# Kernel optimization log

Measured on AMD Instinct MI355X. Metric: run time of the kernel, lower is better.

The kernel has to match this reference:

```python
import jax, jax.numpy as jnp
import numpy as np

B, L, D, N_HEADS = 4, 8192, 1024, 16
HD = D // N_HEADS
MASK_NEG = -1e10


def setup_inputs() -> dict:
    key = jax.random.key(0)
    ks = jax.random.split(key, 5)
    # xavier_normal std for square Dense: sqrt(2/(fan_in+fan_out))
    std = (2.0 / (D + D)) ** 0.5
    return {
        "query": jax.random.normal(ks[0], (B, L, D), dtype=jnp.float32),
        "mask": jax.random.bernoulli(ks[1], 0.1, (B, L)),  # True = masked out
        "Wq": std * jax.random.normal(ks[2], (D, D), dtype=jnp.float32),
        "bq": jnp.zeros((D,), dtype=jnp.float32),
        "Wk": std * jax.random.normal(ks[3], (D, D), dtype=jnp.float32),
        "bk": jnp.zeros((D,), dtype=jnp.float32),
        "Wv": std * jax.random.normal(ks[4], (D, D), dtype=jnp.float32),
        "bv": jnp.zeros((D,), dtype=jnp.float32),
    }


def reference(query, mask, Wq, bq, Wk, bk, Wv, bv):
    # Self-attention: key = value = query (original falls back when key/value are None)
    q = query @ Wq + bq  # [B, L, D]
    k = query @ Wk + bk
    v = query @ Wv + bv
    # split heads: b l (n h) -> b l n h
    qs = q.reshape(B, L, N_HEADS, HD)
    ks_ = k.reshape(B, L, N_HEADS, HD)
    vs = v.reshape(B, L, N_HEADS, HD)
    m = mask[:, :, None, None]  # [B, L, 1, 1], broadcast over heads & dims
    K = jnp.where(m, MASK_NEG, ks_)
    V = jnp.where(m, 0.0, vs)
    # elu kernel feature map: phi(x) = elu(x) + 1 (elu(-1e10)+1 -> 0 for masked keys)
    phiK = jax.nn.elu(K) + 1.0
    phiQ = jax.nn.elu(qs) + 1.0
    # per-head kv summary: [B, N, HD_k, HD_v]
    kv = jnp.einsum('blnk,blnv->bnkv', phiK, V)
    # FAITHFUL to original einsum 'blk,bkv->blk': sums kv over v, elementwise with phiQ
    kv_sum = kv.sum(-1)  # [B, N, HD]
    out = phiQ * kv_sum[:, None, :, :]  # [B, L, N, HD]
    # combine heads: b l n h -> b l (n h)
    return out.reshape(B, L, D)
```

## Files before the change

### kernel.cpp

```cpp
#include <hip/hip_runtime.h>

typedef unsigned short u16;
typedef unsigned int u32;
typedef __attribute__((ext_vector_type(8))) short s16x8;
typedef __attribute__((ext_vector_type(4))) float f32x4;

#define GAS __attribute__((address_space(1)))
#define LAS __attribute__((address_space(3)))

#define BB 4
#define LL 8192
#define DD 1024
#define NH 16
#define HD 64
#define MROWS (BB * LL)
#define NWBT 2064

__device__ __forceinline__ u16 f2bf(float f) {
  u32 u = __builtin_bit_cast(u32, f);
  u32 r = (u + 0x7FFFu + ((u >> 16) & 1u)) >> 16;
  return (u16)r;
}
__device__ __forceinline__ float bf2f(u32 lo) {
  return __builtin_bit_cast(float, lo << 16);
}

__device__ __forceinline__ void async16(const void* g, void* l) {
  __builtin_amdgcn_global_load_lds((const GAS u32*)g, (LAS u32*)l, 16, 0, 0);
}

__device__ __forceinline__ bool get_mask(const void* mp, int row, int mode) {
  if (mode == 2) return ((const unsigned char*)mp)[row] != 0;
  if (mode == 1) return ((const float*)mp)[row] != 0.f;
  return ((const int*)mp)[row] != 0;
}

__global__ void detect_mask(const u32* __restrict__ m, int* __restrict__ flag) {
  int i = blockIdx.x * 256 + threadIdx.x;
  u32 v = m[i];
  int f = 0;
  if (v == 0x3F800000u) f = 1;
  else if (v > 1u) f = 2;
  if (f) atomicMax(flag, f);
}

__global__ void build_wbt(const float* __restrict__ Wq, const float* __restrict__ Wk,
                          u16* __restrict__ WbT) {
  __shared__ float t[32][33];
  const int n0 = blockIdx.x * 32;
  const int k0 = blockIdx.y * 32;
  const float* W = (n0 >> 10) == 0 ? Wq : Wk;
  const int nloc = n0 & 1023;
  const int tx = threadIdx.x, ty = threadIdx.y;
#pragma unroll
  for (int j = 0; j < 32; j += 8)
    t[ty + j][tx] = W[(size_t)(k0 + ty + j) * DD + nloc + tx];
  __syncthreads();
#pragma unroll
  for (int j = 0; j < 32; j += 8)
    WbT[(size_t)(n0 + ty + j) * DD + k0 + tx] = f2bf(t[tx][ty + j]);
}

__global__ void build_wvs(const float* __restrict__ Wv, u16* __restrict__ WbT) {
  int i = blockIdx.x * 256 + threadIdx.x;
  int k = i >> 4, h = i & 15;
  float s = 0.f;
  const float* p = Wv + (size_t)k * DD + h * HD;
#pragma unroll 8
  for (int j = 0; j < 64; ++j) s += p[j];
  WbT[(size_t)(2048 + h) * DD + k] = f2bf(s);
}

__global__ void build_bcat(const float* __restrict__ bq, const float* __restrict__ bk,
                           const float* __restrict__ bv, float* __restrict__ bcat) {
  int i = blockIdx.x * 256 + threadIdx.x;
  if (i < 1024) bcat[i] = bq[i];
  else if (i < 2048) bcat[i] = bk[i - 1024];
  else if (i < 2064) {
    float s = 0.f;
    const float* p = bv + (i - 2048) * HD;
#pragma unroll 8
    for (int j = 0; j < 64; ++j) s += p[j];
    bcat[i] = s;
  }
}

__global__ __launch_bounds__(256) void prep_q(
    const float* __restrict__ query, const u16* __restrict__ WbT,
    const float* __restrict__ bcat, const void* __restrict__ maskp,
    const int* __restrict__ mmode,
    u16* __restrict__ qb, float* __restrict__ sV) {
  __shared__ u16 ldsW[16 * 1024];
  __shared__ u16 ldsA[128 * 64];
  const int tid = threadIdx.x;
  const int lane = tid & 63;
  const int w = tid >> 6;
  const int row0 = blockIdx.x * 128;

  {
    const int h = tid & 15;
    const int cb = tid >> 4;
#pragma unroll
    for (int j = 0; j < 8; ++j) {
      const int c = cb * 8 + j;
      s16x8 v = *(const s16x8*)(WbT + (size_t)(2048 + h) * DD + c * 8);
      *(s16x8*)(ldsW + h * 1024 + (c ^ (h & 7)) * 8) = v;
    }
  }

  const int r_l = tid >> 3;
  const int slot = tid & 7;
  f32x4 acc[2] = {};

  for (int k0 = 0; k0 < DD; k0 += 64) {
    __syncthreads();
#pragma unroll
    for (int i = 0; i < 4; ++i) {
      const int rl = i * 32 + r_l;
      const int seg = slot ^ (rl & 7);
      const float* gp = query + (size_t)(row0 + rl) * DD + k0 + seg * 8;
      float4 v0 = *(const float4*)gp;
      float4 v1 = *(const float4*)(gp + 4);
      s16x8 o;
      o[0] = (short)f2bf(v0.x); o[1] = (short)f2bf(v0.y);
      o[2] = (short)f2bf(v0.z); o[3] = (short)f2bf(v0.w);
      o[4] = (short)f2bf(v1.x); o[5] = (short)f2bf(v1.y);
      o[6] = (short)f2bf(v1.z); o[7] = (short)f2bf(v1.w);
      *(s16x8*)(qb + (size_t)(row0 + rl) * DD + k0 + seg * 8) = o;
      *(s16x8*)(ldsA + rl * 64 + slot * 8) = o;
    }
    __syncthreads();
#pragma unroll
    for (int kk = 0; kk < 2; ++kk) {
      const int segk = kk * 4 + (lane >> 4);
      const int hh = lane & 15;
      const int cc = (k0 >> 3) + segk;
      s16x8 bfr = *(const s16x8*)(ldsW + hh * 1024 + (cc ^ (hh & 7)) * 8);
#pragma unroll
      for (int mi = 0; mi < 2; ++mi) {
        const int r = w * 32 + mi * 16 + hh;
        s16x8 af = *(const s16x8*)(ldsA + r * 64 + ((segk ^ (r & 7))) * 8);
        acc[mi] = __builtin_amdgcn_mfma_f32_16x16x32_bf16(af, bfr, acc[mi], 0, 0, 0);
      }
    }
  }

  const int mode = *mmode;
  const int lanec = lane & 15, laneq = lane >> 4;
#pragma unroll
  for (int mi = 0; mi < 2; ++mi)
#pragma unroll
    for (int r = 0; r < 4; ++r) {
      const int row = row0 + w * 32 + mi * 16 + laneq * 4 + r;
      const bool msk = get_mask(maskp, row, mode);
      float v = acc[mi][r] + bcat[2048 + lanec];
      sV[(size_t)row * NH + lanec] = msk ? 0.f : v;
    }
}

#define BUFSZ 8192
#define UOFF(buf, mat, ks) (((((buf)*2 + (mat))*2 + (ks))) * BUFSZ)

__global__ __launch_bounds__(512, 2) void gemm_qkv(
    const u16* __restrict__ qb, const u16* __restrict__ WbT,
    const float* __restrict__ bcat, const void* __restrict__ maskp,
    const int* __restrict__ mmode,
    const float* __restrict__ sV, float* __restrict__ kv,
    float* __restrict__ out, int phase) {
  __shared__ __align__(16) u16 lds[65536];
  const int tid = threadIdx.x;
  const int lane = tid & 63;
  const int w = tid >> 6;
  const int wm = w & 1, wn = w >> 1;
  const int l15 = lane & 15, l16 = lane >> 4;

  const int bid = blockIdx.x;
  const int swz = (bid & 7) * 64 + (bid >> 3);
  const int mt = swz >> 2;
  const int nt = swz & 3;
  const int row0 = mt * 256;
  const int col0 = (phase ? 1024 : 0) + nt * 256;

  f32x4 acc[8][4] = {};

#define STAGE(buf, mat, ks, kt) do {                                        \
    const u16* gb_ = (mat) ? (WbT + (size_t)col0 * DD)                      \
                           : (qb + (size_t)row0 * DD);                      \
    const int kt_ = (kt) & 15;                                              \
    _Pragma("unroll")                                                       \
    for (int j_ = 0; j_ < 2; ++j_) {                                        \
      int li_ = tid + j_ * 512;                                             \
      int row_ = li_ >> 2, slot_ = li_ & 3;                                 \
      int c_ = slot_ ^ ((row_ >> 1) & 3);                                   \
      async16(gb_ + (size_t)row_ * DD + kt_ * 64 + (ks) * 32 + c_ * 8,      \
              lds + UOFF(buf, mat, ks) + li_ * 8);                          \
    }                                                                       \
  } while (0)

#define LDA(buf, ks, a) do {                                                \
    _Pragma("unroll")                                                       \
    for (int mi_ = 0; mi_ < 8; ++mi_) {                                     \
      int r_ = wm * 128 + mi_ * 16 + l15;                                   \
      a[mi_] = *(const s16x8*)(lds + UOFF(buf, 0, ks) + r_ * 32 +           \
                               ((l16 ^ ((r_ >> 1) & 3)) * 8));              \
    }                                                                       \
  } while (0)

#define LDB2(buf, ks, nb, b) do {                                           \
    _Pragma("unroll")                                                       \
    for (int q_ = 0; q_ < 2; ++q_) {                                        \
      int r_ = wn * 64 + ((nb)*2 + q_) * 16 + l15;                          \
      b[q_] = *(const s16x8*)(lds + UOFF(buf, 1, ks) + r_ * 32 +            \
                              ((l16 ^ ((r_ >> 1) & 3)) * 8));               \
    }                                                                       \
  } while (0)

#define MM(a, b, nb) do {                                                   \
    __builtin_amdgcn_s_setprio(1);                                          \
    _Pragma("unroll")                                                       \
    for (int mi_ = 0; mi_ < 8; ++mi_) {                                     \
      acc[mi_][(nb)*2] = __builtin_amdgcn_mfma_f32_16x16x32_bf16(           \
          a[mi_], b[0], acc[mi_][(nb)*2], 0, 0, 0);                         \
      acc[mi_][(nb)*2 + 1] = __builtin_amdgcn_mfma_f32_16x16x32_bf16(       \
          a[mi_], b[1], acc[mi_][(nb)*2 + 1], 0, 0, 0);                     \
    }                                                                       \
    __builtin_amdgcn_s_setprio(0);                                          \
  } while (0)

#define BAR() __builtin_amdgcn_s_barrier()
#define VMW6() asm volatile("s_waitcnt vmcnt(6)" ::: "memory")

  STAGE(0, 0, 0, 0); STAGE(0, 1, 0, 0); STAGE(0, 0, 1, 0); STAGE(0, 1, 1, 0);
  STAGE(1, 0, 0, 1); STAGE(1, 1, 0, 1); STAGE(1, 0, 1, 1);
  VMW6();
  BAR();

  for (int t = 0; t < 16; t += 2) {
    s16x8 a[8], b[2];
    LDA(0, 0, a); LDB2(0, 0, 0, b);
    STAGE(1, 1, 1, t + 1);
    BAR(); MM(a, b, 0); BAR();
    LDB2(0, 0, 1, b);
    STAGE(0, 0, 0, t + 2);
    BAR(); MM(a, b, 1); BAR();
    LDA(0, 1, a); LDB2(0, 1, 0, b);
    STAGE(0, 1, 0, t + 2);
    BAR(); MM(a, b, 0); BAR();
    LDB2(0, 1, 1, b);
    STAGE(0, 0, 1, t + 2);
    BAR(); MM(a, b, 1); VMW6(); BAR();
    LDA(1, 0, a); LDB2(1, 0, 0, b);
    STAGE(0, 1, 1, t + 2);
    BAR(); MM(a, b, 0); BAR();
    LDB2(1, 0, 1, b);
    STAGE(1, 0, 0, t + 3);
    BAR(); MM(a, b, 1); BAR();
    LDA(1, 1, a); LDB2(1, 1, 0, b);
    STAGE(1, 1, 0, t + 3);
    BAR(); MM(a, b, 0); BAR();
    LDB2(1, 1, 1, b);
    STAGE(1, 0, 1, t + 3);
    BAR(); MM(a, b, 1); VMW6(); BAR();
  }

  const int mode = *mmode;
  const int lanec = lane & 15, laneq = lane >> 4;
  const int wcol0 = col0 + wn * 64;
  const int b_ = row0 >> 13;

  if (phase == 1) {
    const int n = (wcol0 - 1024) >> 6;
    float pc[4] = {0.f, 0.f, 0.f, 0.f};
#pragma unroll
    for (int mi = 0; mi < 8; ++mi) {
#pragma unroll
      for (int r = 0; r < 4; ++r) {
        const int row = row0 + wm * 128 + mi * 16 + laneq * 4 + r;
        const bool msk = get_mask(maskp, row, mode);
        if (!msk) {
          const float sv = sV[(size_t)row * NH + n];
#pragma unroll
          for (int ni = 0; ni < 4; ++ni) {
            const int col = wcol0 + ni * 16 + lanec;
            float v = acc[mi][ni][r] + bcat[col];
            float phi = v > 0.f ? v + 1.f : __expf(v);
            pc[ni] += phi * sv;
          }
        }
      }
    }
#pragma unroll
    for (int ni = 0; ni < 4; ++ni) {
      pc[ni] += __shfl_xor(pc[ni], 16);
      pc[ni] += __shfl_xor(pc[ni], 32);
    }
    if (laneq == 0) {
#pragma unroll
      for (int ni = 0; ni < 4; ++ni) {
        const int colk = wcol0 - 1024 + ni * 16 + lanec;
        atomicAdd(&kv[b_ * DD + colk], pc[ni]);
      }
    }
  } else {
    float kvv[4];
#pragma unroll
    for (int ni = 0; ni < 4; ++ni)
      kvv[ni] = kv[b_ * DD + wcol0 + ni * 16 + lanec];
#pragma unroll
    for (int mi = 0; mi < 8; ++mi) {
#pragma unroll
      for (int r = 0; r < 4; ++r) {
        const int row = row0 + wm * 128 + mi * 16 + laneq * 4 + r;
#pragma unroll
        for (int ni = 0; ni < 4; ++ni) {
          const int col = wcol0 + ni * 16 + lanec;
          float v = acc[mi][ni][r] + bcat[col];
          float phi = v > 0.f ? v + 1.f : __expf(v);
          out[(size_t)row * DD + col] = phi * kvv[ni];
        }
      }
    }
  }
}

extern "C" void kernel_launch(void* const* d_in, const int* in_sizes, int n_in,
                              void* d_out, int out_size, void* d_ws, size_t ws_size,
                              hipStream_t stream) {
  const float* query = (const float*)d_in[0];
  const void* maskp = d_in[1];
  const float* Wq = (const float*)d_in[2];
  const float* bq = (const float*)d_in[3];
  const float* Wk = (const float*)d_in[4];
  const float* bk = (const float*)d_in[5];
  const float* Wv = (const float*)d_in[6];
  const float* bv = (const float*)d_in[7];
  float* out = (float*)d_out;

  char* ws = (char*)d_ws;
  u16* qb = (u16*)ws;            ws += (size_t)MROWS * DD * 2;
  u16* WbT = (u16*)ws;           ws += (size_t)NWBT * DD * 2;
  float* sV = (float*)ws;        ws += (size_t)MROWS * NH * 4;
  float* bcat = (float*)ws;      ws += (size_t)NWBT * 4;
  float* kv = (float*)ws;        ws += (size_t)BB * DD * 4;
  int* mflag = (int*)ws;         ws += 256;

  hipMemsetAsync(kv, 0, (size_t)BB * DD * 4 + 256, stream);

  detect_mask<<<32, 256, 0, stream>>>((const u32*)maskp, mflag);
  build_wbt<<<dim3(2048 / 32, DD / 32), dim3(32, 8), 0, stream>>>(Wq, Wk, WbT);
  build_wvs<<<64, 256, 0, stream>>>(Wv, WbT);
  build_bcat<<<(NWBT + 255) / 256, 256, 0, stream>>>(bq, bk, bv, bcat);
  prep_q<<<MROWS / 128, 256, 0, stream>>>(query, WbT, bcat, maskp, mflag, qb, sV);
  gemm_qkv<<<512, 512, 0, stream>>>(qb, WbT, bcat, maskp, mflag, sV, kv, out, 1);
  gemm_qkv<<<512, 512, 0, stream>>>(qb, WbT, bcat, maskp, mflag, sV, kv, out, 0);
}
```

Baseline: 429.4 us.

## Merge small setup kernels into one launch and halve prep_q tile rows

Combines the mask-type detection, Wv head-sum and bias concatenation kernels into a single build_aux launch that dispatches on block index, cutting two kernel launches. prep_q now processes 64 rows per block instead of 128, which doubles the grid to 512 blocks and gives each wave one MFMA accumulator instead of two. This aims for more parallelism and less launch overhead in the prep phase, at the cost of loading the Wv-sum weights into LDS twice as many times across the grid.

```diff
diff --git a/kernel.cpp b/kernel.cpp
--- a/kernel.cpp
+++ b/kernel.cpp
@@ -33,15 +33,6 @@
   if (mode == 2) return ((const unsigned char*)mp)[row] != 0;
   if (mode == 1) return ((const float*)mp)[row] != 0.f;
   return ((const int*)mp)[row] != 0;
-}
-
-__global__ void detect_mask(const u32* __restrict__ m, int* __restrict__ flag) {
-  int i = blockIdx.x * 256 + threadIdx.x;
-  u32 v = m[i];
-  int f = 0;
-  if (v == 0x3F800000u) f = 1;
-  else if (v > 1u) f = 2;
-  if (f) atomicMax(flag, f);
 }
 
 __global__ void build_wbt(const float* __restrict__ Wq, const float* __restrict__ Wk,
@@ -61,27 +52,39 @@
     WbT[(size_t)(n0 + ty + j) * DD + k0 + tx] = f2bf(t[tx][ty + j]);
 }
 
-__global__ void build_wvs(const float* __restrict__ Wv, u16* __restrict__ WbT) {
-  int i = blockIdx.x * 256 + threadIdx.x;
-  int k = i >> 4, h = i & 15;
-  float s = 0.f;
-  const float* p = Wv + (size_t)k * DD + h * HD;
-#pragma unroll 8
-  for (int j = 0; j < 64; ++j) s += p[j];
-  WbT[(size_t)(2048 + h) * DD + k] = f2bf(s);
-}
-
-__global__ void build_bcat(const float* __restrict__ bq, const float* __restrict__ bk,
-                           const float* __restrict__ bv, float* __restrict__ bcat) {
-  int i = blockIdx.x * 256 + threadIdx.x;
-  if (i < 1024) bcat[i] = bq[i];
-  else if (i < 2048) bcat[i] = bk[i - 1024];
-  else if (i < 2064) {
+__global__ void build_aux(const float* __restrict__ Wv, const float* __restrict__ bq,
+                          const float* __restrict__ bk, const float* __restrict__ bv,
+                          const u32* __restrict__ m,
+                          u16* __restrict__ WbT, float* __restrict__ bcat,
+                          int* __restrict__ flag) {
+  const int blk = blockIdx.x;
+  const int tid = threadIdx.x;
+  if (blk < 64) {
+    int i = blk * 256 + tid;
+    int k = i >> 4, h = i & 15;
     float s = 0.f;
-    const float* p = bv + (i - 2048) * HD;
+    const float* p = Wv + (size_t)k * DD + h * HD;
 #pragma unroll 8
     for (int j = 0; j < 64; ++j) s += p[j];
-    bcat[i] = s;
+    WbT[(size_t)(2048 + h) * DD + k] = f2bf(s);
+  } else if (blk < 73) {
+    int i = (blk - 64) * 256 + tid;
+    if (i < 1024) bcat[i] = bq[i];
+    else if (i < 2048) bcat[i] = bk[i - 1024];
+    else if (i < 2064) {
+      float s = 0.f;
+      const float* p = bv + (i - 2048) * HD;
+#pragma unroll 8
+      for (int j = 0; j < 64; ++j) s += p[j];
+      bcat[i] = s;
+    }
+  } else {
+    int i = (blk - 73) * 256 + tid;
+    u32 v = m[i];
+    int f = 0;
+    if (v == 0x3F800000u) f = 1;
+    else if (v > 1u) f = 2;
+    if (f) atomicMax(flag, f);
   }
 }
 
@@ -91,34 +94,30 @@
     const int* __restrict__ mmode,
     u16* __restrict__ qb, float* __restrict__ sV) {
   __shared__ u16 ldsW[16 * 1024];
-  __shared__ u16 ldsA[128 * 64];
+  __shared__ u16 ldsA[64 * 64];
   const int tid = threadIdx.x;
   const int lane = tid & 63;
   const int w = tid >> 6;
-  const int row0 = blockIdx.x * 128;
-
-  {
-    const int h = tid & 15;
-    const int cb = tid >> 4;
-#pragma unroll
-    for (int j = 0; j < 8; ++j) {
-      const int c = cb * 8 + j;
-      s16x8 v = *(const s16x8*)(WbT + (size_t)(2048 + h) * DD + c * 8);
-      *(s16x8*)(ldsW + h * 1024 + (c ^ (h & 7)) * 8) = v;
-    }
-  }
-
-  const int r_l = tid >> 3;
-  const int slot = tid & 7;
-  f32x4 acc[2] = {};
-
+  const int l15 = lane & 15, l16 = lane >> 4;
+  const int row0 = blockIdx.x * 64;
+
+#pragma unroll
+  for (int j = 0; j < 8; ++j) {
+    int idx = tid + j * 256;
+    int h = idx >> 7, c = idx & 127;
+    s16x8 v = *(const s16x8*)(WbT + (size_t)(2048 + h) * DD + c * 8);
+    *(s16x8*)(ldsW + h * 1024 + (c ^ (h & 7)) * 8) = v;
+  }
+
+  f32x4 acc = {};
   for (int k0 = 0; k0 < DD; k0 += 64) {
     __syncthreads();
 #pragma unroll
-    for (int i = 0; i < 4; ++i) {
-      const int rl = i * 32 + r_l;
-      const int seg = slot ^ (rl & 7);
-      const float* gp = query + (size_t)(row0 + rl) * DD + k0 + seg * 8;
+    for (int j = 0; j < 2; ++j) {
+      int li = tid + j * 256;
+      int row = li >> 3, slot = li & 7;
+      int seg = slot ^ (row & 7);
+      const float* gp = query + (size_t)(row0 + row) * DD + k0 + seg * 8;
       float4 v0 = *(const float4*)gp;
       float4 v1 = *(const float4*)(gp + 4);
       s16x8 o;
@@ -126,36 +125,29 @@
       o[2] = (short)f2bf(v0.z); o[3] = (short)f2bf(v0.w);
       o[4] = (short)f2bf(v1.x); o[5] = (short)f2bf(v1.y);
       o[6] = (short)f2bf(v1.z); o[7] = (short)f2bf(v1.w);
-      *(s16x8*)(qb + (size_t)(row0 + rl) * DD + k0 + seg * 8) = o;
-      *(s16x8*)(ldsA + rl * 64 + slot * 8) = o;
+      *(s16x8*)(qb + (size_t)(row0 + row) * DD + k0 + seg * 8) = o;
+      *(s16x8*)(ldsA + row * 64 + slot * 8) = o;
     }
     __syncthreads();
 #pragma unroll
     for (int kk = 0; kk < 2; ++kk) {
-      const int segk = kk * 4 + (lane >> 4);
-      const int hh = lane & 15;
+      const int segk = kk * 4 + l16;
+      const int r = w * 16 + l15;
+      s16x8 af = *(const s16x8*)(ldsA + r * 64 + ((segk ^ (r & 7))) * 8);
       const int cc = (k0 >> 3) + segk;
-      s16x8 bfr = *(const s16x8*)(ldsW + hh * 1024 + (cc ^ (hh & 7)) * 8);
-#pragma unroll
-      for (int mi = 0; mi < 2; ++mi) {
-        const int r = w * 32 + mi * 16 + hh;
-        s16x8 af = *(const s16x8*)(ldsA + r * 64 + ((segk ^ (r & 7))) * 8);
-        acc[mi] = __builtin_amdgcn_mfma_f32_16x16x32_bf16(af, bfr, acc[mi], 0, 0, 0);
-      }
+      s16x8 bfr = *(const s16x8*)(ldsW + l15 * 1024 + ((cc ^ (l15 & 7))) * 8);
+      acc = __builtin_amdgcn_mfma_f32_16x16x32_bf16(af, bfr, acc, 0, 0, 0);
     }
   }
 
   const int mode = *mmode;
-  const int lanec = lane & 15, laneq = lane >> 4;
-#pragma unroll
-  for (int mi = 0; mi < 2; ++mi)
-#pragma unroll
-    for (int r = 0; r < 4; ++r) {
-      const int row = row0 + w * 32 + mi * 16 + laneq * 4 + r;
-      const bool msk = get_mask(maskp, row, mode);
-      float v = acc[mi][r] + bcat[2048 + lanec];
-      sV[(size_t)row * NH + lanec] = msk ? 0.f : v;
-    }
+#pragma unroll
+  for (int r = 0; r < 4; ++r) {
+    const int row = row0 + w * 16 + l16 * 4 + r;
+    const bool msk = get_mask(maskp, row, mode);
+    float v = acc[r] + bcat[2048 + l15];
+    sV[(size_t)row * NH + l15] = msk ? 0.f : v;
+  }
 }
 
 #define BUFSZ 8192
@@ -346,11 +338,9 @@
 
   hipMemsetAsync(kv, 0, (size_t)BB * DD * 4 + 256, stream);
 
-  detect_mask<<<32, 256, 0, stream>>>((const u32*)maskp, mflag);
   build_wbt<<<dim3(2048 / 32, DD / 32), dim3(32, 8), 0, stream>>>(Wq, Wk, WbT);
-  build_wvs<<<64, 256, 0, stream>>>(Wv, WbT);
-  build_bcat<<<(NWBT + 255) / 256, 256, 0, stream>>>(bq, bk, bv, bcat);
-  prep_q<<<MROWS / 128, 256, 0, stream>>>(query, WbT, bcat, maskp, mflag, qb, sV);
+  build_aux<<<105, 256, 0, stream>>>(Wv, bq, bk, bv, (const u32*)maskp, WbT, bcat, mflag);
+  prep_q<<<MROWS / 64, 256, 0, stream>>>(query, WbT, bcat, maskp, mflag, qb, sV);
   gemm_qkv<<<512, 512, 0, stream>>>(qb, WbT, bcat, maskp, mflag, sV, kv, out, 1);
   gemm_qkv<<<512, 512, 0, stream>>>(qb, WbT, bcat, maskp, mflag, sV, kv, out, 0);
 }
```

Measured after the change: 418.2 us. 1.03x faster.
